# Kernel optimization log

Hardware: AMD Instinct MI355X
Metric: run time of the kernel (lower is better)

The kernel has to match this reference:

```python
import jax, jax.numpy as jnp
import numpy as np

T = 64      # num_time_steps
N = 2048    # nodes
D = 512     # input_dim == hid_dim == out_dim (required by code's residual/split structure)
WEIGHT = 0.5  # residual blend weight from __init__
NEG_BIG = -2.0**32 + 1.0


def setup_inputs() -> dict:
    key = jax.random.key(0)
    ks = jax.random.split(key, 7)
    s = 1.0 / np.sqrt(D)
    return {
        "inputs": jax.random.normal(ks[0], (T, N, D), dtype=jnp.float32),  # stacked snapshots [T,N,F]
        "pos_emb": jax.random.normal(ks[1], (T, D), dtype=jnp.float32) * s,
        "Wq": jax.random.normal(ks[2], (D, D), dtype=jnp.float32) * s,
        "Wk": jax.random.normal(ks[3], (D, D), dtype=jnp.float32) * s,
        "Wv": jax.random.normal(ks[4], (D, D), dtype=jnp.float32) * s,
        "lin_w": jax.random.normal(ks[5], (D, D), dtype=jnp.float32) * s,  # nn.Linear weight [out,in]
        "lin_b": jax.random.normal(ks[6], (D,), dtype=jnp.float32) * 0.01,
    }


def reference(inputs, pos_emb, Wq, Wk, Wv, lin_w, lin_b):
    # stack + permute(1,0,2): [T,N,D] -> [N,T,D]
    x = jnp.transpose(inputs, (1, 0, 2))
    # position embedding gathered by arange(T), broadcast over nodes
    temporal = x + pos_emb[None, :, :]                      # [N,T,D]
    q = jnp.einsum('ntd,de->nte', temporal, Wq)             # [N,T,D]
    k = jnp.einsum('ntd,de->nte', temporal, Wk)
    v = jnp.einsum('ntd,de->nte', temporal, Wv)
    scores = jnp.einsum('nqd,nkd->nqk', q, k)               # [N,T,T] (no sqrt(d) scaling, as in source)
    causal = jnp.tril(jnp.ones((T, T), dtype=bool))
    scores = jnp.where(causal[None], scores, jnp.float32(NEG_BIG))
    attn = jax.nn.softmax(scores, axis=2)                   # dropout inactive (eval mode)
    out = jnp.einsum('nqk,nkd->nqd', attn, v)               # [N,T,D]
    # n_heads == 1: split along dim0 + concat along dim2 is the identity
    ff = jax.nn.relu(jnp.einsum('ntd,ed->nte', out, lin_w) + lin_b) + out
    return WEIGHT * ff + temporal                           # residual=True
```

## Files before the change

### kernel.cpp

```cpp
#include <hip/hip_runtime.h>


#define TT 64
#define NN 2048
#define DD 512

typedef _Float16 f16x8 __attribute__((ext_vector_type(8)));
typedef float    f32x4 __attribute__((ext_vector_type(4)));

#define MFMA16(a,b,c) __builtin_amdgcn_mfma_f32_16x16x32_f16((a),(b),(c),0,0,0)

#define RAW_BARRIER() do { \
    asm volatile("s_waitcnt lgkmcnt(0)" ::: "memory"); \
    __builtin_amdgcn_s_barrier(); \
    __builtin_amdgcn_sched_barrier(0); \
  } while (0)

__global__ __launch_bounds__(256) void prep_weights(
    const float* __restrict__ Wq, const float* __restrict__ Wk,
    const float* __restrict__ Wv, const float* __restrict__ lw,
    _Float16* __restrict__ out)
{
  int gid = blockIdx.x * 256 + threadIdx.x;
  int mat = gid >> 15;
  int r   = gid & 32767;
  int tile = r >> 6;
  int l    = r & 63;
  int rowblk = tile >> 4;
  int kbb    = tile & 15;
  int e  = rowblk * 16 + (l & 15);
  int d0 = kbb * 32 + (l >> 4) * 8;
  union { _Float16 h[8]; uint4 u; } o;
  if (mat < 3) {
    const float* W = (mat == 0) ? Wq : (mat == 1) ? Wk : Wv;
    #pragma unroll
    for (int j = 0; j < 8; ++j)
      o.h[j] = (_Float16)W[(size_t)(d0 + j) * DD + e];
  } else {
    #pragma unroll
    for (int j = 0; j < 8; ++j)
      o.h[j] = (_Float16)lw[(size_t)e * DD + d0 + j];
  }
  *(uint4*)(out + (size_t)gid * 8) = o.u;
}

__global__ __launch_bounds__(512) void attn_fused(
    const float* __restrict__ x, const float* __restrict__ pos,
    const _Float16* __restrict__ WF, _Float16* __restrict__ outp)
{
  __shared__ char smem[54272];
  char* const tst0 = smem;
  char* const tst1 = smem + 5120;
  char* const qdp  = smem + 10240;
  char* const scb  = smem + 10240;
  char* const vdp  = smem + 10240;
  char* const kdp  = smem + 27648;
  char* const atn  = smem + 45056;

  const int n    = blockIdx.x;
  const int tid  = threadIdx.x;
  const int wid  = tid >> 6;
  const int lane = tid & 63;
  const int quad = lane >> 4;
  const int l15  = lane & 15;
  const size_t scrbase = (size_t)n * 65536 + 32768;

  const _Float16* const Fq = WF;
  const _Float16* const Fk = WF + 262144;
  const _Float16* const Fv = WF + 524288;

  const int srow = tid >> 3, si = tid & 7;
  auto t_issue = [&](int kb, f32x4& xv, f32x4& pv) {
    xv = *(const f32x4*)(x + ((size_t)srow * NN + n) * DD + kb * 32 + 4 * si);
    pv = *(const f32x4*)(pos + (size_t)srow * DD + kb * 32 + 4 * si);
  };
  auto t_store = [&](char* buf, const f32x4& xv, const f32x4& pv) {
    union { _Float16 h[4]; unsigned long long u; } o;
    #pragma unroll
    for (int j = 0; j < 4; ++j) o.h[j] = (_Float16)(xv[j] + pv[j]);
    *(unsigned long long*)(buf + srow * 80 + 8 * si) = o.u;
  };

  f32x4 sacc[2] = {};

  for (int ph = 0; ph < 2; ++ph) {
    f32x4 acc[4][4] = {};
    const bool isK = (wid >= 4);
    const int  esl = wid & 3;
    const _Float16* const fwave =
        (isK ? Fk : Fq) + (size_t)(ph * 16 + esl * 4) * 8192 + (size_t)lane * 8;

    {
      f32x4 xa, pa;
      t_issue(0, xa, pa);
      t_store(tst0, xa, pa);
    }
    char* tcur = tst0; char* tnxt = tst1;
    for (int kb = 0; kb < 16; ++kb) {
      f16x8 bf[4];
      #pragma unroll
      for (int ct = 0; ct < 4; ++ct)
        bf[ct] = *(const f16x8*)(fwave + (size_t)kb * 512 + (size_t)ct * 8192);
      f32x4 xb, pb;
      if (kb < 15) t_issue(kb + 1, xb, pb);
      RAW_BARRIER();
      f16x8 af[4];
      #pragma unroll
      for (int rt = 0; rt < 4; ++rt)
        af[rt] = *(const f16x8*)(tcur + (16 * rt + l15) * 80 + quad * 16);
      #pragma unroll
      for (int ct = 0; ct < 4; ++ct)
        #pragma unroll
        for (int rt = 0; rt < 4; ++rt)
          acc[rt][ct] = MFMA16(af[rt], bf[ct], acc[rt][ct]);
      if (kb < 15) t_store(tnxt, xb, pb);
      char* t = tcur; tcur = tnxt; tnxt = t;
    }

    for (int r = 0; r < 2; ++r) {
      __syncthreads();
      if ((esl >> 1) == r) {
        char* dst = isK ? kdp : qdp;
        const int colbase = (esl & 1) * 64;
        #pragma unroll
        for (int rt = 0; rt < 4; ++rt)
          #pragma unroll
          for (int ct = 0; ct < 4; ++ct)
            #pragma unroll
            for (int rg = 0; rg < 4; ++rg)
              *(_Float16*)(dst + (16*rt + quad*4 + rg)*272 + (colbase + 16*ct + l15)*2)
                  = (_Float16)acc[rt][ct][rg];
      }
      __syncthreads();
      const int srt = wid >> 1, sct0 = (wid & 1) * 2;
      #pragma unroll
      for (int ks = 0; ks < 4; ++ks) {
        f16x8 aq = *(const f16x8*)(qdp + (16*srt + l15)*272 + ks*64 + quad*16);
        #pragma unroll
        for (int j = 0; j < 2; ++j) {
          f16x8 bk = *(const f16x8*)(kdp + (16*(sct0+j) + l15)*272 + ks*64 + quad*16);
          sacc[j] = MFMA16(aq, bk, sacc[j]);
        }
      }
    }
  }

  __syncthreads();
  {
    const int srt = wid >> 1, sct0 = (wid & 1) * 2;
    #pragma unroll
    for (int j = 0; j < 2; ++j)
      #pragma unroll
      for (int rg = 0; rg < 4; ++rg)
        *(float*)(scb + (16*srt + quad*4 + rg)*272 + (16*(sct0+j) + l15)*4) = sacc[j][rg];
  }
  __syncthreads();
  {
    const int row = tid >> 3, i = tid & 7;
    f32x4 s0 = *(const f32x4*)(scb + row*272 + 32*i);
    f32x4 s1 = *(const f32x4*)(scb + row*272 + 32*i + 16);
    float s[8] = { s0[0],s0[1],s0[2],s0[3], s1[0],s1[1],s1[2],s1[3] };
    float m = -3.0e38f;
    #pragma unroll
    for (int j = 0; j < 8; ++j) if (8*i + j <= row) m = fmaxf(m, s[j]);
    m = fmaxf(m, __shfl_xor(m, 1));
    m = fmaxf(m, __shfl_xor(m, 2));
    m = fmaxf(m, __shfl_xor(m, 4));
    float e[8]; float sum = 0.f;
    #pragma unroll
    for (int j = 0; j < 8; ++j) {
      e[j] = (8*i + j <= row) ? __expf(s[j] - m) : 0.f;
      sum += e[j];
    }
    sum += __shfl_xor(sum, 1);
    sum += __shfl_xor(sum, 2);
    sum += __shfl_xor(sum, 4);
    const float inv = 1.0f / sum;
    union { _Float16 h[8]; uint4 u; } o;
    #pragma unroll
    for (int j = 0; j < 8; ++j) o.h[j] = (_Float16)(e[j] * inv);
    *(uint4*)(atn + row*144 + 16*i) = o.u;
  }

  f32x4 vacc[4][4] = {};
  {
    const _Float16* const fwv = Fv + (size_t)(wid * 4) * 8192 + (size_t)lane * 8;
    {
      f32x4 xa, pa;
      t_issue(0, xa, pa);
      t_store(tst0, xa, pa);
    }
    char* tcur = tst0; char* tnxt = tst1;
    for (int kb = 0; kb < 16; ++kb) {
      f16x8 bf[4];
      #pragma unroll
      for (int ct = 0; ct < 4; ++ct)
        bf[ct] = *(const f16x8*)(fwv + (size_t)kb * 512 + (size_t)ct * 8192);
      f32x4 xb, pb;
      if (kb < 15) t_issue(kb + 1, xb, pb);
      RAW_BARRIER();
      f16x8 af[4];
      #pragma unroll
      for (int rt = 0; rt < 4; ++rt)
        af[rt] = *(const f16x8*)(tcur + (16 * rt + l15) * 80 + quad * 16);
      #pragma unroll
      for (int ct = 0; ct < 4; ++ct)
        #pragma unroll
        for (int rt = 0; rt < 4; ++rt)
          vacc[rt][ct] = MFMA16(af[rt], bf[ct], vacc[rt][ct]);
      if (kb < 15) t_store(tnxt, xb, pb);
      char* t = tcur; tcur = tnxt; tnxt = t;
    }
  }

  __syncthreads();
  char* const vd = vdp + wid * 4352;
  #pragma unroll
  for (int h = 0; h < 2; ++h) {
    #pragma unroll
    for (int c = 0; c < 2; ++c) {
      const int ct = 2*h + c;
      #pragma unroll
      for (int rt = 0; rt < 4; ++rt)
        #pragma unroll
        for (int rg = 0; rg < 4; ++rg)
          *(_Float16*)(vd + (16*c + l15)*136 + (16*rt + quad*4 + rg)*2)
              = (_Float16)vacc[rt][ct][rg];
    }
    f32x4 oacc[2][4] = {};
    #pragma unroll
    for (int ks = 0; ks < 2; ++ks) {
      f16x8 av[2];
      #pragma unroll
      for (int mt = 0; mt < 2; ++mt)
        av[mt] = *(const f16x8*)(vd + (16*mt + l15)*136 + ks*64 + quad*16);
      #pragma unroll
      for (int nt = 0; nt < 4; ++nt) {
        f16x8 ba = *(const f16x8*)(atn + (16*nt + l15)*144 + ks*64 + quad*16);
        #pragma unroll
        for (int mt = 0; mt < 2; ++mt)
          oacc[mt][nt] = MFMA16(av[mt], ba, oacc[mt][nt]);
      }
    }
    #pragma unroll
    for (int mt = 0; mt < 2; ++mt)
      #pragma unroll
      for (int nt = 0; nt < 4; ++nt) {
        const int d0 = 64*wid + 32*h + 16*mt + quad*4;
        const int tq = 16*nt + l15;
        union { _Float16 h4[4]; uint2 u; } o;
        #pragma unroll
        for (int rg = 0; rg < 4; ++rg) o.h4[rg] = (_Float16)oacc[mt][nt][rg];
        *(uint2*)(outp + scrbase + (size_t)tq * DD + d0) = o.u;
      }
  }
}

__global__ __launch_bounds__(512) void ff_final(
    const _Float16* outp, const float* __restrict__ x,
    const float* __restrict__ pos, const _Float16* __restrict__ lwF,
    const float* __restrict__ lb, float* y)
{
  __shared__ char smem[10240];
  char* const ost0 = smem;
  char* const ost1 = smem + 5120;

  const int n = blockIdx.x;
  const int tid = threadIdx.x;
  const int wid = tid >> 6, lane = tid & 63, quad = lane >> 4, l15 = lane & 15;
  const size_t scrbase = (size_t)n * 65536 + 32768;

  const _Float16* const fA = lwF + (size_t)(wid * 4) * 8192 + (size_t)lane * 8;

  const int srow = tid >> 3, si = tid & 7;
  auto o_issue = [&](int kb, unsigned long long& v) {
    v = *(const unsigned long long*)(outp + scrbase + (size_t)srow * DD + kb * 32 + 4 * si);
  };
  auto o_store = [&](char* buf, unsigned long long v) {
    *(unsigned long long*)(buf + srow * 80 + 8 * si) = v;
  };

  f32x4 acc[4][4] = {};
  {
    unsigned long long va;
    o_issue(0, va);
    o_store(ost0, va);
  }
  char* ocur = ost0; char* onxt = ost1;
  for (int kb = 0; kb < 16; ++kb) {
    f16x8 af[4];
    #pragma unroll
    for (int mt = 0; mt < 4; ++mt)
      af[mt] = *(const f16x8*)(fA + (size_t)kb * 512 + (size_t)mt * 8192);
    unsigned long long vb = 0;
    if (kb < 15) o_issue(kb + 1, vb);
    RAW_BARRIER();
    #pragma unroll
    for (int nt = 0; nt < 4; ++nt) {
      f16x8 bo = *(const f16x8*)(ocur + (16 * nt + l15) * 80 + quad * 16);
      #pragma unroll
      for (int mt = 0; mt < 4; ++mt)
        acc[mt][nt] = MFMA16(af[mt], bo, acc[mt][nt]);
    }
    if (kb < 15) o_store(onxt, vb);
    char* t = ocur; ocur = onxt; onxt = t;
  }

  uint2 ovv[4][4];
  #pragma unroll
  for (int mt = 0; mt < 4; ++mt) {
    const int e0 = wid*64 + 16*mt + quad*4;
    #pragma unroll
    for (int nt = 0; nt < 4; ++nt) {
      const int tq = 16*nt + l15;
      ovv[mt][nt] = *(const uint2*)(outp + scrbase + (size_t)tq * DD + e0);
    }
  }
  __syncthreads();

  #pragma unroll
  for (int mt = 0; mt < 4; ++mt) {
    const int e0 = wid*64 + 16*mt + quad*4;
    f32x4 bias = *(const f32x4*)(lb + e0);
    #pragma unroll
    for (int nt = 0; nt < 4; ++nt) {
      const int tq = 16*nt + l15;
      const size_t base = ((size_t)n * TT + tq) * DD + e0;
      union { _Float16 h4[4]; uint2 u; } ov;
      ov.u = ovv[mt][nt];
      f32x4 xv = *(const f32x4*)(x + ((size_t)tq * NN + n) * DD + e0);
      f32x4 pv = *(const f32x4*)(pos + (size_t)tq * DD + e0);
      f32x4 ro;
      #pragma unroll
      for (int rg = 0; rg < 4; ++rg) {
        float ff = acc[mt][nt][rg] + bias[rg];
        ff = ff > 0.f ? ff : 0.f;
        ro[rg] = 0.5f * (ff + (float)ov.h4[rg]) + xv[rg] + pv[rg];
      }
      *(f32x4*)(y + base) = ro;
    }
  }
}

extern "C" void kernel_launch(void* const* d_in, const int* in_sizes, int n_in,
                              void* d_out, int out_size, void* d_ws, size_t ws_size,
                              hipStream_t stream) {
  (void)in_sizes; (void)n_in; (void)out_size; (void)ws_size;
  const float* x   = (const float*)d_in[0];
  const float* pos = (const float*)d_in[1];
  const float* Wq  = (const float*)d_in[2];
  const float* Wk  = (const float*)d_in[3];
  const float* Wv  = (const float*)d_in[4];
  const float* lw  = (const float*)d_in[5];
  const float* lb  = (const float*)d_in[6];
  _Float16* wsW = (_Float16*)d_ws;

  prep_weights<<<512, 256, 0, stream>>>(Wq, Wk, Wv, lw, wsW);
  attn_fused<<<2048, 512, 0, stream>>>(x, pos, wsW, (_Float16*)d_out);
  ff_final<<<2048, 512, 0, stream>>>((const _Float16*)d_out, x, pos,
                                     wsW + 786432, lb, (float*)d_out);
}
```

Baseline: 1.006 ms.

## Stage full per-node fp16 tiles in swizzled LDS once instead of streaming

In attn_fused, the whole 64x512 (x+pos) tile is converted to fp16 and stored in LDS once, using an XOR swizzle. The Q/K and V projection loops then read it without per-step barriers, and x and pos are no longer re-read from global memory for each of the three projection passes. ff_final likewise loads the whole attention-output tile into swizzled LDS up front and reuses it for the residual term instead of re-reading global scratch. This removes per-iteration barriers and redundant global traffic. The cost is much larger LDS use (about 107KB and 64KB per block), which lowers occupancy and removes the load/compute overlap of the old double buffering.

```diff
diff --git a/kernel.cpp b/kernel.cpp
--- a/kernel.cpp
+++ b/kernel.cpp
@@ -9,12 +9,6 @@
 typedef float    f32x4 __attribute__((ext_vector_type(4)));
 
 #define MFMA16(a,b,c) __builtin_amdgcn_mfma_f32_16x16x32_f16((a),(b),(c),0,0,0)
-
-#define RAW_BARRIER() do { \
-    asm volatile("s_waitcnt lgkmcnt(0)" ::: "memory"); \
-    __builtin_amdgcn_s_barrier(); \
-    __builtin_amdgcn_sched_barrier(0); \
-  } while (0)
 
 __global__ __launch_bounds__(256) void prep_weights(
     const float* __restrict__ Wq, const float* __restrict__ Wk,
@@ -48,14 +42,13 @@
     const float* __restrict__ x, const float* __restrict__ pos,
     const _Float16* __restrict__ WF, _Float16* __restrict__ outp)
 {
-  __shared__ char smem[54272];
-  char* const tst0 = smem;
-  char* const tst1 = smem + 5120;
-  char* const qdp  = smem + 10240;
-  char* const scb  = smem + 10240;
-  char* const vdp  = smem + 10240;
-  char* const kdp  = smem + 27648;
-  char* const atn  = smem + 45056;
+  __shared__ char smem[109568];
+  char* const tstp = smem;
+  char* const qdp  = smem + 65536;
+  char* const scb  = smem + 65536;
+  char* const vdp  = smem + 65536;
+  char* const kdp  = smem + 82944;
+  char* const atn  = smem + 100352;
 
   const int n    = blockIdx.x;
   const int tid  = threadIdx.x;
@@ -69,18 +62,25 @@
   const _Float16* const Fk = WF + 262144;
   const _Float16* const Fv = WF + 524288;
 
-  const int srow = tid >> 3, si = tid & 7;
-  auto t_issue = [&](int kb, f32x4& xv, f32x4& pv) {
-    xv = *(const f32x4*)(x + ((size_t)srow * NN + n) * DD + kb * 32 + 4 * si);
-    pv = *(const f32x4*)(pos + (size_t)srow * DD + kb * 32 + 4 * si);
-  };
-  auto t_store = [&](char* buf, const f32x4& xv, const f32x4& pv) {
-    union { _Float16 h[4]; unsigned long long u; } o;
-    #pragma unroll
-    for (int j = 0; j < 4; ++j) o.h[j] = (_Float16)(xv[j] + pv[j]);
-    *(unsigned long long*)(buf + srow * 80 + 8 * si) = o.u;
-  };
-
+  {
+    const int row = tid >> 3, si = tid & 7;
+    const float* xr = x + ((size_t)row * NN + n) * DD;
+    const float* pr = pos + (size_t)row * DD;
+    char* const dst = tstp + row * 1024;
+    const int swz = (row & 7) << 4;
+    #pragma unroll
+    for (int kb = 0; kb < 16; ++kb) {
+      f32x4 xv = *(const f32x4*)(xr + kb * 32 + 4 * si);
+      f32x4 pv = *(const f32x4*)(pr + kb * 32 + 4 * si);
+      union { _Float16 h[4]; unsigned long long u; } o;
+      #pragma unroll
+      for (int j = 0; j < 4; ++j) o.h[j] = (_Float16)(xv[j] + pv[j]);
+      *(unsigned long long*)(dst + ((kb * 64 + si * 8) ^ swz)) = o.u;
+    }
+  }
+  __syncthreads();
+
+  const int rswz = (l15 & 7) << 4;
   f32x4 sacc[2] = {};
 
   for (int ph = 0; ph < 2; ++ph) {
@@ -90,31 +90,22 @@
     const _Float16* const fwave =
         (isK ? Fk : Fq) + (size_t)(ph * 16 + esl * 4) * 8192 + (size_t)lane * 8;
 
-    {
-      f32x4 xa, pa;
-      t_issue(0, xa, pa);
-      t_store(tst0, xa, pa);
-    }
-    char* tcur = tst0; char* tnxt = tst1;
+    #pragma unroll
     for (int kb = 0; kb < 16; ++kb) {
       f16x8 bf[4];
       #pragma unroll
       for (int ct = 0; ct < 4; ++ct)
         bf[ct] = *(const f16x8*)(fwave + (size_t)kb * 512 + (size_t)ct * 8192);
-      f32x4 xb, pb;
-      if (kb < 15) t_issue(kb + 1, xb, pb);
-      RAW_BARRIER();
       f16x8 af[4];
       #pragma unroll
       for (int rt = 0; rt < 4; ++rt)
-        af[rt] = *(const f16x8*)(tcur + (16 * rt + l15) * 80 + quad * 16);
+        af[rt] = *(const f16x8*)(tstp + (16 * rt + l15) * 1024 +
+                                 ((kb * 64 + quad * 16) ^ rswz));
       #pragma unroll
       for (int ct = 0; ct < 4; ++ct)
         #pragma unroll
         for (int rt = 0; rt < 4; ++rt)
           acc[rt][ct] = MFMA16(af[rt], bf[ct], acc[rt][ct]);
-      if (kb < 15) t_store(tnxt, xb, pb);
-      char* t = tcur; tcur = tnxt; tnxt = t;
     }
 
     for (int r = 0; r < 2; ++r) {
@@ -185,31 +176,22 @@
   f32x4 vacc[4][4] = {};
   {
     const _Float16* const fwv = Fv + (size_t)(wid * 4) * 8192 + (size_t)lane * 8;
-    {
-      f32x4 xa, pa;
-      t_issue(0, xa, pa);
-      t_store(tst0, xa, pa);
-    }
-    char* tcur = tst0; char* tnxt = tst1;
+    #pragma unroll
     for (int kb = 0; kb < 16; ++kb) {
       f16x8 bf[4];
       #pragma unroll
       for (int ct = 0; ct < 4; ++ct)
         bf[ct] = *(const f16x8*)(fwv + (size_t)kb * 512 + (size_t)ct * 8192);
-      f32x4 xb, pb;
-      if (kb < 15) t_issue(kb + 1, xb, pb);
-      RAW_BARRIER();
       f16x8 af[4];
       #pragma unroll
       for (int rt = 0; rt < 4; ++rt)
-        af[rt] = *(const f16x8*)(tcur + (16 * rt + l15) * 80 + quad * 16);
+        af[rt] = *(const f16x8*)(tstp + (16 * rt + l15) * 1024 +
+                                 ((kb * 64 + quad * 16) ^ rswz));
       #pragma unroll
       for (int ct = 0; ct < 4; ++ct)
         #pragma unroll
         for (int rt = 0; rt < 4; ++rt)
           vacc[rt][ct] = MFMA16(af[rt], bf[ct], vacc[rt][ct]);
-      if (kb < 15) t_store(tnxt, xb, pb);
-      char* t = tcur; tcur = tnxt; tnxt = t;
     }
   }
 
@@ -257,66 +239,48 @@
 }
 
 __global__ __launch_bounds__(512) void ff_final(
-    const _Float16* outp, const float* __restrict__ x,
+    const _Float16* __restrict__ outp, const float* __restrict__ x,
     const float* __restrict__ pos, const _Float16* __restrict__ lwF,
-    const float* __restrict__ lb, float* y)
+    const float* __restrict__ lb, float* __restrict__ y)
 {
-  __shared__ char smem[10240];
-  char* const ost0 = smem;
-  char* const ost1 = smem + 5120;
+  __shared__ char smem[65536];
 
   const int n = blockIdx.x;
   const int tid = threadIdx.x;
   const int wid = tid >> 6, lane = tid & 63, quad = lane >> 4, l15 = lane & 15;
   const size_t scrbase = (size_t)n * 65536 + 32768;
 
+  {
+    const int row = tid >> 3, si = tid & 7;
+    const _Float16* sr = outp + scrbase + (size_t)row * DD;
+    char* const dst = smem + row * 1024;
+    const int swz = (row & 7) << 4;
+    #pragma unroll
+    for (int kb = 0; kb < 16; ++kb)
+      *(unsigned long long*)(dst + ((kb * 64 + si * 8) ^ swz)) =
+          *(const unsigned long long*)(sr + kb * 32 + 4 * si);
+  }
+  __syncthreads();
+
+  const int rswz = (l15 & 7) << 4;
   const _Float16* const fA = lwF + (size_t)(wid * 4) * 8192 + (size_t)lane * 8;
 
-  const int srow = tid >> 3, si = tid & 7;
-  auto o_issue = [&](int kb, unsigned long long& v) {
-    v = *(const unsigned long long*)(outp + scrbase + (size_t)srow * DD + kb * 32 + 4 * si);
-  };
-  auto o_store = [&](char* buf, unsigned long long v) {
-    *(unsigned long long*)(buf + srow * 80 + 8 * si) = v;
-  };
-
   f32x4 acc[4][4] = {};
-  {
-    unsigned long long va;
-    o_issue(0, va);
-    o_store(ost0, va);
-  }
-  char* ocur = ost0; char* onxt = ost1;
+  #pragma unroll
   for (int kb = 0; kb < 16; ++kb) {
     f16x8 af[4];
     #pragma unroll
     for (int mt = 0; mt < 4; ++mt)
       af[mt] = *(const f16x8*)(fA + (size_t)kb * 512 + (size_t)mt * 8192);
-    unsigned long long vb = 0;
-    if (kb < 15) o_issue(kb + 1, vb);
-    RAW_BARRIER();
     #pragma unroll
     for (int nt = 0; nt < 4; ++nt) {
-      f16x8 bo = *(const f16x8*)(ocur + (16 * nt + l15) * 80 + quad * 16);
+      f16x8 bo = *(const f16x8*)(smem + (16 * nt + l15) * 1024 +
+                                 ((kb * 64 + quad * 16) ^ rswz));
       #pragma unroll
       for (int mt = 0; mt < 4; ++mt)
         acc[mt][nt] = MFMA16(af[mt], bo, acc[mt][nt]);
     }
-    if (kb < 15) o_store(onxt, vb);
-    char* t = ocur; ocur = onxt; onxt = t;
-  }
-
-  uint2 ovv[4][4];
-  #pragma unroll
-  for (int mt = 0; mt < 4; ++mt) {
-    const int e0 = wid*64 + 16*mt + quad*4;
-    #pragma unroll
-    for (int nt = 0; nt < 4; ++nt) {
-      const int tq = 16*nt + l15;
-      ovv[mt][nt] = *(const uint2*)(outp + scrbase + (size_t)tq * DD + e0);
-    }
-  }
-  __syncthreads();
+  }
 
   #pragma unroll
   for (int mt = 0; mt < 4; ++mt) {
@@ -326,8 +290,8 @@
     for (int nt = 0; nt < 4; ++nt) {
       const int tq = 16*nt + l15;
       const size_t base = ((size_t)n * TT + tq) * DD + e0;
-      union { _Float16 h4[4]; uint2 u; } ov;
-      ov.u = ovv[mt][nt];
+      union { _Float16 h4[4]; unsigned long long u; } ov;
+      ov.u = *(const unsigned long long*)(smem + tq * 1024 + ((2 * e0) ^ rswz));
       f32x4 xv = *(const f32x4*)(x + ((size_t)tq * NN + n) * DD + e0);
       f32x4 pv = *(const f32x4*)(pos + (size_t)tq * DD + e0);
       f32x4 ro;
```

Result: faster. 953.5 us (-5.2%).
